# Kernel tuning notes

Measured on AMD Instinct MI355X. Metric: run time of the kernel, lower is better.

## Reference

```python
import jax, jax.numpy as jnp
import numpy as np

T = 1.0  # temperature (init kwarg t)
N, M, D = 16384, 16384, 64


def setup_inputs() -> dict:
    key = jax.random.key(0)
    k1, k2, k3 = jax.random.split(key, 3)
    logits = jax.random.normal(k1, (N, D), dtype=jnp.float32)
    targets = jax.random.normal(k2, (M, D), dtype=jnp.float32)
    # probabilities in (0,1]; bounded away from 0 so log is finite
    noise_probs = jax.random.uniform(k3, (D,), dtype=jnp.float32, minval=1e-3, maxval=1.0)
    return {"logits": logits, "targets": targets, "noise_probs": noise_probs}


def reference(logits, targets, noise_probs):
    # q: (N, d) = logits / t - log(noise_probs)
    q = logits / T - jnp.log(noise_probs)[None, :]
    # The torch repeat/unsqueeze/reshape broadcast-multiply-sum is exactly a GEMM:
    # scores[n, m] = sum_d q[n, d] * targets[m, d]
    scores = jnp.einsum('nd,md->nm', q, targets)  # (N, M)
    # subtract detached row max (numerical stabilization, no grad through max)
    scores = scores - jax.lax.stop_gradient(jnp.max(scores, axis=1, keepdims=True))
    # CrossEntropyLoss with labels = arange(N) (non-distributed path), mean reduction
    logp = jax.nn.log_softmax(scores, axis=1)  # (N, M)
    labels = jnp.arange(scores.shape[0])
    picked = jnp.take_along_axis(logp, labels[:, None], axis=1)[:, 0]  # (N,)
    return -jnp.mean(picked)
```

## Files before the change

kernel.cpp:

```cpp
#include <hip/hip_runtime.h>
#include <stdint.h>

#define N_ROWS 16384
#define NSPLIT 16
#define COLS_PER_SPLIT (N_ROWS / NSPLIT)
#define N_ITER (COLS_PER_SPLIT / 64)
#define SHIFT2 64.0f
#define LOG2E 1.44269504088896340736f
#define LN2 0.69314718055994530942f
#define POISON_U32 0xAAAAAAAAu

using short8  = __attribute__((ext_vector_type(8))) short;
using float4v = __attribute__((ext_vector_type(4))) float;

__device__ __forceinline__ unsigned short f2bf(float f) {
  unsigned u = __float_as_uint(f);
  unsigned r = (u + 0x7fffu + ((u >> 16) & 1u)) >> 16;
  return (unsigned short)r;
}
__device__ __forceinline__ float bf2f(unsigned short s) {
  return __uint_as_float(((unsigned)s) << 16);
}

__device__ __forceinline__ void async_stage_16(const void* g, void* l) {
  __builtin_amdgcn_global_load_lds(
      (const __attribute__((address_space(1))) uint32_t*)g,
      (__attribute__((address_space(3))) uint32_t*)l, 16, 0, 0);
}

__device__ __forceinline__ void stage_tile64(const uint8_t* gbase, uint8_t* lds,
                                             int wave, int lane) {
#pragma unroll
  for (int q = 0; q < 2; ++q) {
    int t = wave * 2 + q;
    int row = t * 8 + (lane >> 3);
    int c = (lane & 7) ^ (row & 7);
    async_stage_16(gbase + row * 128 + c * 16, lds + t * 1024 + lane * 16);
  }
}

__global__ void prep_kernel(const float4* __restrict__ lg,
                            const float4* __restrict__ tg,
                            const float* __restrict__ noise,
                            ushort4* __restrict__ qa,
                            ushort4* __restrict__ tb,
                            float* __restrict__ diag) {
  int tid = threadIdx.x;
  int i = blockIdx.x * blockDim.x + tid;
  int d4 = (i & 15) << 2;
  float4 l = lg[i];
  float4 t = tg[i];
  ushort4 ua, ub;
  ua.x = f2bf(l.x * LOG2E - log2f(noise[d4 + 0]));
  ua.y = f2bf(l.y * LOG2E - log2f(noise[d4 + 1]));
  ua.z = f2bf(l.z * LOG2E - log2f(noise[d4 + 2]));
  ua.w = f2bf(l.w * LOG2E - log2f(noise[d4 + 3]));
  ub.x = f2bf(t.x);
  ub.y = f2bf(t.y);
  ub.z = f2bf(t.z);
  ub.w = f2bf(t.w);
  qa[i] = ua;
  tb[i] = ub;

  float part = bf2f(ua.x) * bf2f(ub.x) + bf2f(ua.y) * bf2f(ub.y) +
               bf2f(ua.z) * bf2f(ub.z) + bf2f(ua.w) * bf2f(ub.w);
  part += __shfl_xor(part, 1);
  part += __shfl_xor(part, 2);
  part += __shfl_xor(part, 4);
  part += __shfl_xor(part, 8);
  if ((tid & 15) == 0) diag[i >> 4] = part;
}

__global__ __launch_bounds__(256, 3) void flash_kernel(
    const uint8_t* __restrict__ qa,
    const uint8_t* __restrict__ tb,
    const float* __restrict__ diag,
    float* __restrict__ row_sums,
    unsigned* __restrict__ cnt,
    unsigned* __restrict__ done_cnt,
    float* __restrict__ ws_loss,
    float* __restrict__ out) {
  __shared__ __align__(16) uint8_t ldsB0[64 * 128];
  __shared__ __align__(16) uint8_t ldsB1[64 * 128];
  __shared__ int is_last;

  const int bid = blockIdx.x;
  const int rb = bid >> 4;
  const int sp = bid & 15;
  const int tid = threadIdx.x;
  const int wave = tid >> 6;
  const int lane = tid & 63;
  const int m = lane & 15;
  const int kc = lane >> 4;

  const int row0 = rb * 128;
  const int col0 = sp * COLS_PER_SPLIT;
  const int rows_off = wave * 32;

  stage_tile64(tb + (size_t)col0 * 128, ldsB0, wave, lane);

  short8 afrag[2][2];
#pragma unroll
  for (int i = 0; i < 2; ++i)
#pragma unroll
    for (int k2 = 0; k2 < 2; ++k2)
      afrag[i][k2] = *(const short8*)(qa +
          (size_t)(row0 + rows_off + i * 16 + m) * 128 + (k2 * 4 + kc) * 16);

  float sums[2][4];
#pragma unroll
  for (int i = 0; i < 2; ++i)
#pragma unroll
    for (int r = 0; r < 4; ++r) sums[i][r] = 0.f;

  __syncthreads();

  auto do_tile = [&](const uint8_t* buf) {
    short8 bfrag[4][2];
#pragma unroll
    for (int j = 0; j < 4; ++j)
#pragma unroll
      for (int k2 = 0; k2 < 2; ++k2) {
        int r = j * 16 + m;
        int c = (k2 * 4 + kc) ^ (r & 7);
        bfrag[j][k2] = *(const short8*)(buf + r * 128 + c * 16);
      }
#pragma unroll
    for (int j = 0; j < 4; ++j) {
      float4v acc[2];
#pragma unroll
      for (int i = 0; i < 2; ++i) {
        float4v a0 = {-SHIFT2, -SHIFT2, -SHIFT2, -SHIFT2};
        a0 = __builtin_amdgcn_mfma_f32_16x16x32_bf16(afrag[i][0], bfrag[j][0], a0, 0, 0, 0);
        a0 = __builtin_amdgcn_mfma_f32_16x16x32_bf16(afrag[i][1], bfrag[j][1], a0, 0, 0, 0);
        acc[i] = a0;
      }
#pragma unroll
      for (int i = 0; i < 2; ++i)
#pragma unroll
        for (int r = 0; r < 4; ++r)
          sums[i][r] += __builtin_amdgcn_exp2f(acc[i][r]);
    }
  };

  for (int it2 = 0; it2 < N_ITER / 2; ++it2) {
    int t0 = it2 * 2;
    stage_tile64(tb + (size_t)(col0 + (t0 + 1) * 64) * 128, ldsB1, wave, lane);
    do_tile(ldsB0);
    __syncthreads();
    if (t0 + 2 < N_ITER)
      stage_tile64(tb + (size_t)(col0 + (t0 + 2) * 64) * 128, ldsB0, wave, lane);
    do_tile(ldsB1);
    __syncthreads();
  }

#pragma unroll
  for (int i = 0; i < 2; ++i)
#pragma unroll
    for (int r = 0; r < 4; ++r) {
      float v = sums[i][r];
      v += __shfl_xor(v, 1);
      v += __shfl_xor(v, 2);
      v += __shfl_xor(v, 4);
      v += __shfl_xor(v, 8);
      if (m == 0) {
        int grow = row0 + rows_off + i * 16 + kc * 4 + r;
        atomicAdd(&row_sums[grow], v);
      }
    }

  __syncthreads();
  if (tid == 0) {
    unsigned old = atomicAdd(&cnt[rb], 1u);
    is_last = (old == POISON_U32 + (NSPLIT - 1)) ? 1 : 0;
  }
  __syncthreads();

  if (is_last) {
    float part = 0.f;
    if (tid < 128) {
      int n = row0 + tid;
      float s = atomicAdd(&row_sums[n], 0.0f);
      part = LN2 * (SHIFT2 + log2f(s) - diag[n]);
    }
    part += __shfl_xor(part, 1);
    part += __shfl_xor(part, 2);
    part += __shfl_xor(part, 4);
    part += __shfl_xor(part, 8);
    part += __shfl_xor(part, 16);
    part += __shfl_xor(part, 32);
    if (tid < 128 && lane == 0) atomicAdd(ws_loss, part);
    __syncthreads();
    if (tid == 0) {
      unsigned old2 = atomicAdd(done_cnt, 1u);
      if (old2 == POISON_U32 + 127u) {
        float tot = atomicAdd(ws_loss, 0.0f);
        out[0] = tot * (1.0f / N_ROWS);
      }
    }
  }
}

extern "C" void kernel_launch(void* const* d_in, const int* in_sizes, int n_in,
                              void* d_out, int out_size, void* d_ws, size_t ws_size,
                              hipStream_t stream) {
  const float* logits  = (const float*)d_in[0];
  const float* targets = (const float*)d_in[1];
  const float* noise   = (const float*)d_in[2];
  float* out = (float*)d_out;

  uint8_t* ws = (uint8_t*)d_ws;
  uint8_t* qa = ws;
  uint8_t* tb = ws + (size_t)2 * 1024 * 1024;
  float* diag         = (float*)(ws + (size_t)4 * 1024 * 1024);
  float* row_sums     = (float*)(ws + (size_t)4 * 1024 * 1024 + 65536);
  unsigned* cnt       = (unsigned*)(ws + (size_t)4 * 1024 * 1024 + 131072);
  unsigned* done_cnt  = (unsigned*)(ws + (size_t)4 * 1024 * 1024 + 131072 + 512);
  float* ws_loss      = (float*)(ws + (size_t)4 * 1024 * 1024 + 131072 + 516);

  prep_kernel<<<1024, 256, 0, stream>>>(
      (const float4*)logits, (const float4*)targets, noise,
      (ushort4*)qa, (ushort4*)tb, diag);

  flash_kernel<<<128 * NSPLIT, 256, 0, stream>>>(
      qa, tb, diag, row_sums, cnt, done_cnt, ws_loss, out);
}
```

Measured before the change: 107.5 us.

## Fuse bf16 conversion and diagonal computation into flash kernel, drop prep launch

```diff
diff --git a/kernel.cpp b/kernel.cpp
--- a/kernel.cpp
+++ b/kernel.cpp
@@ -13,68 +13,20 @@
 using short8  = __attribute__((ext_vector_type(8))) short;
 using float4v = __attribute__((ext_vector_type(4))) float;
 
-__device__ __forceinline__ unsigned short f2bf(float f) {
-  unsigned u = __float_as_uint(f);
-  unsigned r = (u + 0x7fffu + ((u >> 16) & 1u)) >> 16;
-  return (unsigned short)r;
-}
 __device__ __forceinline__ float bf2f(unsigned short s) {
   return __uint_as_float(((unsigned)s) << 16);
 }
-
-__device__ __forceinline__ void async_stage_16(const void* g, void* l) {
-  __builtin_amdgcn_global_load_lds(
-      (const __attribute__((address_space(1))) uint32_t*)g,
-      (__attribute__((address_space(3))) uint32_t*)l, 16, 0, 0);
-}
-
-__device__ __forceinline__ void stage_tile64(const uint8_t* gbase, uint8_t* lds,
-                                             int wave, int lane) {
-#pragma unroll
-  for (int q = 0; q < 2; ++q) {
-    int t = wave * 2 + q;
-    int row = t * 8 + (lane >> 3);
-    int c = (lane & 7) ^ (row & 7);
-    async_stage_16(gbase + row * 128 + c * 16, lds + t * 1024 + lane * 16);
-  }
-}
-
-__global__ void prep_kernel(const float4* __restrict__ lg,
-                            const float4* __restrict__ tg,
-                            const float* __restrict__ noise,
-                            ushort4* __restrict__ qa,
-                            ushort4* __restrict__ tb,
-                            float* __restrict__ diag) {
-  int tid = threadIdx.x;
-  int i = blockIdx.x * blockDim.x + tid;
-  int d4 = (i & 15) << 2;
-  float4 l = lg[i];
-  float4 t = tg[i];
-  ushort4 ua, ub;
-  ua.x = f2bf(l.x * LOG2E - log2f(noise[d4 + 0]));
-  ua.y = f2bf(l.y * LOG2E - log2f(noise[d4 + 1]));
-  ua.z = f2bf(l.z * LOG2E - log2f(noise[d4 + 2]));
-  ua.w = f2bf(l.w * LOG2E - log2f(noise[d4 + 3]));
-  ub.x = f2bf(t.x);
-  ub.y = f2bf(t.y);
-  ub.z = f2bf(t.z);
-  ub.w = f2bf(t.w);
-  qa[i] = ua;
-  tb[i] = ub;
-
-  float part = bf2f(ua.x) * bf2f(ub.x) + bf2f(ua.y) * bf2f(ub.y) +
-               bf2f(ua.z) * bf2f(ub.z) + bf2f(ua.w) * bf2f(ub.w);
-  part += __shfl_xor(part, 1);
-  part += __shfl_xor(part, 2);
-  part += __shfl_xor(part, 4);
-  part += __shfl_xor(part, 8);
-  if ((tid & 15) == 0) diag[i >> 4] = part;
+__device__ __forceinline__ uint32_t cvtpk(float lo, float hi) {
+  uint32_t r;
+  asm("v_cvt_pk_bf16_f32 %0, %1, %2" : "=v"(r) : "v"(lo), "v"(hi));
+  return r;
 }
 
 __global__ __launch_bounds__(256, 3) void flash_kernel(
-    const uint8_t* __restrict__ qa,
-    const uint8_t* __restrict__ tb,
-    const float* __restrict__ diag,
+    const float* __restrict__ logits,
+    const float* __restrict__ targets,
+    const float* __restrict__ noise,
+    float* __restrict__ diag,
     float* __restrict__ row_sums,
     unsigned* __restrict__ cnt,
     unsigned* __restrict__ done_cnt,
@@ -84,9 +36,10 @@
   __shared__ __align__(16) uint8_t ldsB1[64 * 128];
   __shared__ int is_last;
 
-  const int bid = blockIdx.x;
-  const int rb = bid >> 4;
-  const int sp = bid & 15;
+  const int bid0 = blockIdx.x;
+  const int bid = (bid0 & 7) * 256 + (bid0 >> 3);
+  const int sp = bid >> 7;
+  const int rb = bid & 127;
   const int tid = threadIdx.x;
   const int wave = tid >> 6;
   const int lane = tid & 63;
@@ -97,23 +50,84 @@
   const int col0 = sp * COLS_PER_SPLIT;
   const int rows_off = wave * 32;
 
-  stage_tile64(tb + (size_t)col0 * 128, ldsB0, wave, lane);
+  const float4v* tg4 = (const float4v*)targets;
+  float4v stg[4];
+  auto issue_loads = [&](int t) {
+#pragma unroll
+    for (int j = 0; j < 4; ++j) {
+      int rr = col0 + t * 64 + wave * 16 + j * 4 + (lane >> 4);
+      stg[j] = tg4[(size_t)rr * 16 + (lane & 15)];
+    }
+  };
+  auto write_stage = [&](uint8_t* buf) {
+#pragma unroll
+    for (int j = 0; j < 4; ++j) {
+      int row = wave * 16 + j * 4 + (lane >> 4);
+      uint64_t v = ((uint64_t)cvtpk(stg[j][2], stg[j][3]) << 32) |
+                   (uint64_t)cvtpk(stg[j][0], stg[j][1]);
+      int cs = ((lane & 15) >> 1) ^ (row & 7);
+      *(uint64_t*)(buf + row * 128 + cs * 16 + (lane & 1) * 8) = v;
+    }
+  };
 
   short8 afrag[2][2];
 #pragma unroll
+  for (int k2 = 0; k2 < 2; ++k2) {
+    const float4v* np = (const float4v*)noise + (size_t)(k2 * 4 + kc) * 2;
+    float4v n0 = np[0], n1 = np[1];
+    float ln[8];
+#pragma unroll
+    for (int z = 0; z < 4; ++z) { ln[z] = __log2f(n0[z]); ln[4 + z] = __log2f(n1[z]); }
+#pragma unroll
+    for (int i = 0; i < 2; ++i) {
+      int row = row0 + rows_off + i * 16 + m;
+      const float4v* lp = (const float4v*)(logits + (size_t)row * 64 + (k2 * 4 + kc) * 8);
+      float4v a = lp[0], b = lp[1];
+      float q[8];
+#pragma unroll
+      for (int z = 0; z < 4; ++z) {
+        q[z]     = a[z] * LOG2E - ln[z];
+        q[4 + z] = b[z] * LOG2E - ln[4 + z];
+      }
+      union { uint32_t u[4]; short8 s; } pk;
+      pk.u[0] = cvtpk(q[0], q[1]); pk.u[1] = cvtpk(q[2], q[3]);
+      pk.u[2] = cvtpk(q[4], q[5]); pk.u[3] = cvtpk(q[6], q[7]);
+      afrag[i][k2] = pk.s;
+    }
+  }
+
+  if (sp == (rb >> 3)) {
+#pragma unroll
+    for (int i = 0; i < 2; ++i) {
+      int row = row0 + rows_off + i * 16 + m;
+      float d = 0.f;
+#pragma unroll
+      for (int k2 = 0; k2 < 2; ++k2) {
+        const float4v* tp = (const float4v*)(targets + (size_t)row * 64 + (k2 * 4 + kc) * 8);
+        float4v ta = tp[0], tb2 = tp[1];
+        uint32_t t01 = cvtpk(ta[0], ta[1]),  t23 = cvtpk(ta[2], ta[3]);
+        uint32_t t45 = cvtpk(tb2[0], tb2[1]), t67 = cvtpk(tb2[2], tb2[3]);
+        union { short8 s; uint32_t u[4]; } q; q.s = afrag[i][k2];
+        d += bf2f((unsigned short)(q.u[0] & 0xffffu)) * bf2f((unsigned short)(t01 & 0xffffu));
+        d += bf2f((unsigned short)(q.u[0] >> 16))     * bf2f((unsigned short)(t01 >> 16));
+        d += bf2f((unsigned short)(q.u[1] & 0xffffu)) * bf2f((unsigned short)(t23 & 0xffffu));
+        d += bf2f((unsigned short)(q.u[1] >> 16))     * bf2f((unsigned short)(t23 >> 16));
+        d += bf2f((unsigned short)(q.u[2] & 0xffffu)) * bf2f((unsigned short)(t45 & 0xffffu));
+        d += bf2f((unsigned short)(q.u[2] >> 16))     * bf2f((unsigned short)(t45 >> 16));
+        d += bf2f((unsigned short)(q.u[3] & 0xffffu)) * bf2f((unsigned short)(t67 & 0xffffu));
+        d += bf2f((unsigned short)(q.u[3] >> 16))     * bf2f((unsigned short)(t67 >> 16));
+      }
+      d += __shfl_xor(d, 16);
+      d += __shfl_xor(d, 32);
+      if (kc == 0) atomicAdd(&diag[row], d);
+    }
+  }
+
+  float sums[2][4];
+#pragma unroll
   for (int i = 0; i < 2; ++i)
 #pragma unroll
-    for (int k2 = 0; k2 < 2; ++k2)
-      afrag[i][k2] = *(const short8*)(qa +
-          (size_t)(row0 + rows_off + i * 16 + m) * 128 + (k2 * 4 + kc) * 16);
-
-  float sums[2][4];
-#pragma unroll
-  for (int i = 0; i < 2; ++i)
-#pragma unroll
     for (int r = 0; r < 4; ++r) sums[i][r] = 0.f;
-
-  __syncthreads();
 
   auto do_tile = [&](const uint8_t* buf) {
     short8 bfrag[4][2];
@@ -127,30 +141,33 @@
       }
 #pragma unroll
     for (int j = 0; j < 4; ++j) {
-      float4v acc[2];
 #pragma unroll
       for (int i = 0; i < 2; ++i) {
         float4v a0 = {-SHIFT2, -SHIFT2, -SHIFT2, -SHIFT2};
         a0 = __builtin_amdgcn_mfma_f32_16x16x32_bf16(afrag[i][0], bfrag[j][0], a0, 0, 0, 0);
         a0 = __builtin_amdgcn_mfma_f32_16x16x32_bf16(afrag[i][1], bfrag[j][1], a0, 0, 0, 0);
-        acc[i] = a0;
-      }
-#pragma unroll
-      for (int i = 0; i < 2; ++i)
 #pragma unroll
         for (int r = 0; r < 4; ++r)
-          sums[i][r] += __builtin_amdgcn_exp2f(acc[i][r]);
+          sums[i][r] += __builtin_amdgcn_exp2f(a0[r]);
+      }
     }
   };
+
+  issue_loads(0);
+  write_stage(ldsB0);
+  __syncthreads();
 
   for (int it2 = 0; it2 < N_ITER / 2; ++it2) {
     int t0 = it2 * 2;
-    stage_tile64(tb + (size_t)(col0 + (t0 + 1) * 64) * 128, ldsB1, wave, lane);
+    issue_loads(t0 + 1);
     do_tile(ldsB0);
     __syncthreads();
-    if (t0 + 2 < N_ITER)
-      stage_tile64(tb + (size_t)(col0 + (t0 + 2) * 64) * 128, ldsB0, wave, lane);
+    write_stage(ldsB1);
+    __syncthreads();
+    if (t0 + 2 < N_ITER) issue_loads(t0 + 2);
     do_tile(ldsB1);
+    __syncthreads();
+    if (t0 + 2 < N_ITER) write_stage(ldsB0);
     __syncthreads();
   }
 
@@ -181,7 +198,8 @@
     if (tid < 128) {
       int n = row0 + tid;
       float s = atomicAdd(&row_sums[n], 0.0f);
-      part = LN2 * (SHIFT2 + log2f(s) - diag[n]);
+      float dg = atomicAdd(&diag[n], 0.0f);
+      part = LN2 * (SHIFT2 + log2f(s) - dg);
     }
     part += __shfl_xor(part, 1);
     part += __shfl_xor(part, 2);
@@ -210,18 +228,12 @@
   float* out = (float*)d_out;
 
   uint8_t* ws = (uint8_t*)d_ws;
-  uint8_t* qa = ws;
-  uint8_t* tb = ws + (size_t)2 * 1024 * 1024;
-  float* diag         = (float*)(ws + (size_t)4 * 1024 * 1024);
-  float* row_sums     = (float*)(ws + (size_t)4 * 1024 * 1024 + 65536);
-  unsigned* cnt       = (unsigned*)(ws + (size_t)4 * 1024 * 1024 + 131072);
-  unsigned* done_cnt  = (unsigned*)(ws + (size_t)4 * 1024 * 1024 + 131072 + 512);
-  float* ws_loss      = (float*)(ws + (size_t)4 * 1024 * 1024 + 131072 + 516);
-
-  prep_kernel<<<1024, 256, 0, stream>>>(
-      (const float4*)logits, (const float4*)targets, noise,
-      (ushort4*)qa, (ushort4*)tb, diag);
+  float* diag         = (float*)ws;
+  float* row_sums     = (float*)(ws + 65536);
+  unsigned* cnt       = (unsigned*)(ws + 131072);
+  unsigned* done_cnt  = (unsigned*)(ws + 131072 + 512);
+  float* ws_loss      = (float*)(ws + 131072 + 516);
 
   flash_kernel<<<128 * NSPLIT, 256, 0, stream>>>(
-      qa, tb, diag, row_sums, cnt, done_cnt, ws_loss, out);
-}
+      logits, targets, noise, diag, row_sums, cnt, done_cnt, ws_loss, out);
+}
```

New measurement: 114.0 us. 6.1% more time.
